# Optimization experiments

Hardware: AMD Instinct MI355X
Metric: run time of the kernel (lower is better)

The kernel has to match this reference:

```python
import jax, jax.numpy as jnp
import numpy as np

NUM_KEYS = 128          # int(sqrt(num_cdmoe_experts)) = sqrt(16384)
TOP_K = 8               # num_cdmoe_experts_per_head
NUM_HEADS = 4           # num_cdmoe_heads


def setup_inputs() -> dict:
    key = jax.random.key(0)
    ks = jax.random.split(key, 8)
    b, t, d = 1, 2048, 1024
    inter = 2048
    E, h, ret = 16384, NUM_HEADS, 64
    s = 0.02
    return {
        "hidden_states": jax.random.normal(ks[0], (b, t, d), jnp.float32),
        "w_queries": jax.random.normal(ks[1], (h * ret, d), jnp.float32) * s,
        "keys": jax.random.normal(ks[2], (h, NUM_KEYS, 2, ret // 2), jnp.float32) * s,
        "down_embed": jax.random.normal(ks[3], (E, d), jnp.float32) * s,
        "up_embed": jax.random.normal(ks[4], (E, d), jnp.float32) * s,
        "w_gate": jax.random.normal(ks[5], (inter, d), jnp.float32) * s,
        "w_up": jax.random.normal(ks[6], (inter, d), jnp.float32) * s,
        "w_down": jax.random.normal(ks[7], (d, inter), jnp.float32) * s,
    }


def reference(hidden_states, w_queries, keys, down_embed, up_embed, w_gate, w_up, w_down):
    b, t, d = hidden_states.shape
    h, nk, _, n = keys.shape  # (heads, num_keys, 2, retrieval_dim//2)
    k = TOP_K

    # query projection, split into the two product-key halves: (b, t, 2, h, n)
    q = (hidden_states @ w_queries.T).reshape(b, t, 2, h, n)
    # sim: (2, b, t, h, num_keys)
    sim = jnp.einsum("btphn,hkpn->pbthk", q, keys)

    # per-codebook top-k
    sx, ix = jax.lax.top_k(sim[0], k)  # (b, t, h, k)
    sy, iy = jax.lax.top_k(sim[1], k)

    # cartesian combine: (b, t, h, k*k)
    all_scores = (sx[..., :, None] + sy[..., None, :]).reshape(b, t, h, k * k)
    all_idx = (ix[..., :, None] * nk + iy[..., None, :]).reshape(b, t, h, k * k)

    scores, pos = jax.lax.top_k(all_scores, k)          # (b, t, h, k)
    indices = jnp.take_along_axis(all_idx, pos, axis=-1)  # expert ids in [0, nk*nk)

    de = down_embed[indices]  # (b, t, h, k, d)
    ue = up_embed[indices]    # (b, t, h, k, d)

    ew = jnp.einsum("btd,bthkd->bthk", hidden_states, de)
    ew = jax.nn.silu(ew) * jax.nn.softmax(scores, axis=-1)
    experts_states = jnp.einsum("bthk,bthkd->btd", ew, ue)

    # dense (inherited DogeMLP) path
    mlp = (jax.nn.silu(hidden_states @ w_gate.T) * (hidden_states @ w_up.T)) @ w_down.T
    return mlp + experts_states
```

## Files before the change

kernel.cpp:

```cpp
#include <hip/hip_runtime.h>
#include <hip/hip_bf16.h>
#include <math.h>


#define TOKENS 2048
#define DIM    1024
#define INTER  2048
#define NKEYS  128
#define TOPK   8
#define HEADS  4
#define NINF  -3.4e38f

typedef unsigned short ushort_t;
typedef __attribute__((ext_vector_type(8))) short bf16x8;
typedef __attribute__((ext_vector_type(4))) float f32x4;

__device__ __forceinline__ float bf2f(ushort_t u) {
    unsigned int x = (unsigned int)u << 16;
    float f; __builtin_memcpy(&f, &x, 4); return f;
}
__device__ __forceinline__ ushort_t f2bf_rne(float f) {
    unsigned int x; __builtin_memcpy(&x, &f, 4);
    x += 0x7fffu + ((x >> 16) & 1u);
    return (ushort_t)(x >> 16);
}
__device__ __forceinline__ void gload_lds16(const void* g, void* l) {
    __builtin_amdgcn_global_load_lds(
        (const __attribute__((address_space(1))) unsigned int*)g,
        (__attribute__((address_space(3))) unsigned int*)l, 16, 0, 0);
}

__global__ __launch_bounds__(256) void convert_all(
    const float* __restrict__ h,  const float* __restrict__ wq,
    const float* __restrict__ wg, const float* __restrict__ wu,
    const float* __restrict__ wd,
    ushort_t* __restrict__ hb,  ushort_t* __restrict__ wqb,
    ushort_t* __restrict__ wgb, ushort_t* __restrict__ wub,
    ushort_t* __restrict__ wdb) {
    const int i = blockIdx.x * 256 + threadIdx.x;
    const float* src; ushort_t* dst; int off;
    if      (i <  262144) { src = h;  dst = hb;  off = i; }
    else if (i <  294912) { src = wq; dst = wqb; off = i - 262144; }
    else if (i <  557056) { src = wg; dst = wgb; off = i - 294912; }
    else if (i <  819200) { src = wu; dst = wub; off = i - 557056; }
    else                  { src = wd; dst = wdb; off = i - 819200; }
    const float4* p = (const float4*)src + (size_t)off * 2;
    const float4 a = p[0], b = p[1];
    uint4 o;
    o.x = (unsigned)f2bf_rne(a.x) | ((unsigned)f2bf_rne(a.y) << 16);
    o.y = (unsigned)f2bf_rne(a.z) | ((unsigned)f2bf_rne(a.w) << 16);
    o.z = (unsigned)f2bf_rne(b.x) | ((unsigned)f2bf_rne(b.y) << 16);
    o.w = (unsigned)f2bf_rne(b.z) | ((unsigned)f2bf_rne(b.w) << 16);
    ((uint4*)dst)[off] = o;
}

template<int BM, int BN, int WR, int WC, int FM, int FN, int EPI>
__global__ __launch_bounds__(256) void mfma_gemm(const ushort_t* __restrict__ A,
                                                 const ushort_t* __restrict__ B,
                                                 const void* __restrict__ extra,
                                                 void* __restrict__ Cout,
                                                 int M, int N, int K) {
    static_assert(WR * WC == 4 && WR * FM * 16 == BM && WC * FN * 16 == BN, "geom");
    __shared__ ushort_t As[BM * 32];
    __shared__ ushort_t Bs[BN * 32];
    const int tid = threadIdx.x;
    const int w = tid >> 6, lane = tid & 63;
    const int wr = w / WC, wc = w % WC;
    const int m0 = blockIdx.y * BM, n0 = blockIdx.x * BN;

    const int srow = (w << 4) + (lane >> 2);
    const int scol = (lane & 3) << 3;
    const ushort_t* Ag = &A[(size_t)(m0 + srow) * K + scol];
    const ushort_t* Bg = &B[(size_t)(n0 + srow) * K + scol];
    ushort_t* Al = &As[w << 9];
    ushort_t* Bl = &Bs[w << 9];

    const int frow = lane & 15;
    const int fcol = (lane >> 4) << 3;
    const ushort_t* Afr = &As[(size_t)(wr * FM * 16 + frow) * 32 + fcol];
    const ushort_t* Bfr = &Bs[(size_t)(wc * FN * 16 + frow) * 32 + fcol];

    f32x4 acc[FM][FN];
#pragma unroll
    for (int i = 0; i < FM; ++i)
#pragma unroll
        for (int j = 0; j < FN; ++j) acc[i][j] = (f32x4){0.f, 0.f, 0.f, 0.f};

    for (int k0 = 0; k0 < K; k0 += 32) {
        __syncthreads();
#pragma unroll
        for (int i = 0; i < BM / 64; ++i)
            gload_lds16(Ag + (size_t)i * 64 * K + k0, Al + i * 2048);
#pragma unroll
        for (int i = 0; i < BN / 64; ++i)
            gload_lds16(Bg + (size_t)i * 64 * K + k0, Bl + i * 2048);
        __syncthreads();

        bf16x8 af[FM], bfv[FN];
#pragma unroll
        for (int i = 0; i < FM; ++i) af[i] = *(const bf16x8*)(Afr + i * 512);
#pragma unroll
        for (int j = 0; j < FN; ++j) bfv[j] = *(const bf16x8*)(Bfr + j * 512);
#pragma unroll
        for (int i = 0; i < FM; ++i)
#pragma unroll
            for (int j = 0; j < FN; ++j)
                acc[i][j] = __builtin_amdgcn_mfma_f32_16x16x32_bf16(
                    af[i], bfv[j], acc[i][j], 0, 0, 0);
    }

    const int crow0 = m0 + wr * FM * 16 + ((lane >> 4) << 2);
    const int ccol0 = n0 + wc * FN * 16 + (lane & 15);
#pragma unroll
    for (int i = 0; i < FM; ++i)
#pragma unroll
        for (int j = 0; j < FN; ++j)
#pragma unroll
            for (int r = 0; r < 4; ++r) {
                const size_t off = (size_t)(crow0 + i * 16 + r) * N + ccol0 + j * 16;
                float v = acc[i][j][r];
                if (EPI == 1) {
                    const float gg = bf2f(((const ushort_t*)extra)[off]);
                    v *= gg / (1.f + __expf(-gg));
                    ((ushort_t*)Cout)[off] = f2bf_rne(v);
                } else if (EPI == 2) {
                    ((float*)Cout)[off] = v + ((const float*)extra)[off];
                } else if (EPI == 3) {
                    ((ushort_t*)Cout)[off] = f2bf_rne(v);
                } else {
                    ((float*)Cout)[off] = v;
                }
            }
}

__global__ __launch_bounds__(256) void silu_mul_inplace(const ushort_t* __restrict__ g,
                                                        ushort_t* __restrict__ u) {
    const int i = blockIdx.x * 256 + threadIdx.x;
    const uint4 gv = ((const uint4*)g)[i];
    const uint4 uv = ((const uint4*)u)[i];
    const unsigned gw[4] = {gv.x, gv.y, gv.z, gv.w};
    const unsigned uw[4] = {uv.x, uv.y, uv.z, uv.w};
    unsigned ow[4];
#pragma unroll
    for (int j = 0; j < 4; ++j) {
        const float g0 = bf2f((ushort_t)(gw[j] & 0xffff));
        const float g1 = bf2f((ushort_t)(gw[j] >> 16));
        const float u0 = bf2f((ushort_t)(uw[j] & 0xffff));
        const float u1 = bf2f((ushort_t)(uw[j] >> 16));
        const float v0 = g0 / (1.f + __expf(-g0)) * u0;
        const float v1 = g1 / (1.f + __expf(-g1)) * u1;
        ow[j] = (unsigned)f2bf_rne(v0) | ((unsigned)f2bf_rne(v1) << 16);
    }
    ((uint4*)u)[i] = (uint4){ow[0], ow[1], ow[2], ow[3]};
}

__device__ __forceinline__ void topk_body(int t, const float* __restrict__ q,
                                          const float* __restrict__ keys,
                                          int* __restrict__ eidx,
                                          float* __restrict__ ewgt) {
    const int head = threadIdx.x >> 6;
    const int lane = threadIdx.x & 63;

    const float4* qx = (const float4*)&q[(size_t)t * 256 + head * 32];
    const float4* qy = (const float4*)&q[(size_t)t * 256 + 128 + head * 32];
    float4 qxv[8], qyv[8];
#pragma unroll
    for (int n = 0; n < 8; ++n) { qxv[n] = qx[n]; qyv[n] = qy[n]; }

    float cx0, cx1, cy0, cy1;
    {
        float s[4];
#pragma unroll
        for (int j = 0; j < 2; ++j) {
            const int k = 2 * lane + j;
            const float4* kx = (const float4*)&keys[(size_t)(((head << 7) | k) * 2 + 0) * 32];
            const float4* ky = (const float4*)&keys[(size_t)(((head << 7) | k) * 2 + 1) * 32];
            float sx = 0.f, sy = 0.f;
#pragma unroll
            for (int n = 0; n < 8; ++n) {
                const float4 a = qxv[n], b = kx[n];
                sx += a.x * b.x + a.y * b.y + a.z * b.z + a.w * b.w;
                const float4 c = qyv[n], d = ky[n];
                sy += c.x * d.x + c.y * d.y + c.z * d.z + c.w * d.w;
            }
            s[j * 2] = sx; s[j * 2 + 1] = sy;
        }
        cx0 = s[0]; cy0 = s[1]; cx1 = s[2]; cy1 = s[3];
    }

    float sx_mine = NINF, sy_mine = NINF;
    int sxi_mine = 0, syi_mine = 0;
    {
        float c0 = cx0, c1 = cx1;
#pragma unroll
        for (int it = 0; it < TOPK; ++it) {
            float bv; int bi;
            if (c1 > c0) { bv = c1; bi = 2 * lane + 1; } else { bv = c0; bi = 2 * lane; }
#pragma unroll
            for (int m = 1; m < 64; m <<= 1) {
                const float ov = __shfl_xor(bv, m);
                const int   oi = __shfl_xor(bi, m);
                if (ov > bv || (ov == bv && oi < bi)) { bv = ov; bi = oi; }
            }
            if (lane == it) { sx_mine = bv; sxi_mine = bi; }
            if (bi == 2 * lane) c0 = NINF;
            else if (bi == 2 * lane + 1) c1 = NINF;
        }
    }
    {
        float c0 = cy0, c1 = cy1;
#pragma unroll
        for (int it = 0; it < TOPK; ++it) {
            float bv; int bi;
            if (c1 > c0) { bv = c1; bi = 2 * lane + 1; } else { bv = c0; bi = 2 * lane; }
#pragma unroll
            for (int m = 1; m < 64; m <<= 1) {
                const float ov = __shfl_xor(bv, m);
                const int   oi = __shfl_xor(bi, m);
                if (ov > bv || (ov == bv && oi < bi)) { bv = ov; bi = oi; }
            }
            if (lane == it) { sy_mine = bv; syi_mine = bi; }
            if (bi == 2 * lane) c0 = NINF;
            else if (bi == 2 * lane + 1) c1 = NINF;
        }
    }

    const float sa = __shfl(sx_mine, lane >> 3);
    const int   ia = __shfl(sxi_mine, lane >> 3);
    const float sb = __shfl(sy_mine, lane & 7);
    const int   ib = __shfl(syi_mine, lane & 7);
    float cv = sa + sb;
    const int ci = ia * NKEYS + ib;

    float fs_mine = NINF; int fi_mine = 0;
#pragma unroll
    for (int it = 0; it < TOPK; ++it) {
        float bv = cv; int bp = lane; int bx = ci;
#pragma unroll
        for (int m = 1; m < 64; m <<= 1) {
            const float ov = __shfl_xor(bv, m);
            const int   op = __shfl_xor(bp, m);
            const int   ox = __shfl_xor(bx, m);
            if (ov > bv || (ov == bv && op < bp)) { bv = ov; bp = op; bx = ox; }
        }
        if (lane == it) { fs_mine = bv; fi_mine = bx; }
        if (lane == bp) cv = NINF;
    }

    float f[8];
#pragma unroll
    for (int j = 0; j < 8; ++j) f[j] = __shfl(fs_mine, j);
    float mx = f[0];
#pragma unroll
    for (int j = 1; j < 8; ++j) mx = fmaxf(mx, f[j]);
    float ssum = 0.f;
#pragma unroll
    for (int j = 0; j < 8; ++j) ssum += expf(f[j] - mx);
    if (lane < 8) {
        eidx[t * 32 + head * 8 + lane] = fi_mine;
        ewgt[t * 32 + head * 8 + lane] = expf(fs_mine - mx) / ssum;
    }
}

__global__ __launch_bounds__(256) void topk_kernel(const float* __restrict__ q,
                                                   const float* __restrict__ keys,
                                                   int* __restrict__ eidx,
                                                   float* __restrict__ ewgt) {
    topk_body(blockIdx.x, q, keys, eidx, ewgt);
}

__global__ __launch_bounds__(256) void topk_conv_kernel(
    const float* __restrict__ q, const float* __restrict__ keys,
    int* __restrict__ eidx, float* __restrict__ ewgt,
    const float* __restrict__ de_f32, const float* __restrict__ ue_f32,
    ushort_t* __restrict__ deb, ushort_t* __restrict__ ueb) {
    const int b = blockIdx.x;
    if (b < TOKENS) {
        topk_body(b, q, keys, eidx, ewgt);
        return;
    }
    const int id = b - TOKENS;
    const float* src = (id < 8192) ? de_f32 : ue_f32;
    ushort_t*    dst = (id < 8192) ? deb : ueb;
    const size_t off = (size_t)(id & 8191) * 2048 + threadIdx.x * 8;
    const float4* p = (const float4*)(src + off);
    const float4 a = p[0], bb = p[1];
    uint4 o;
    o.x = (unsigned)f2bf_rne(a.x)  | ((unsigned)f2bf_rne(a.y)  << 16);
    o.y = (unsigned)f2bf_rne(a.z)  | ((unsigned)f2bf_rne(a.w)  << 16);
    o.z = (unsigned)f2bf_rne(bb.x) | ((unsigned)f2bf_rne(bb.y) << 16);
    o.w = (unsigned)f2bf_rne(bb.z) | ((unsigned)f2bf_rne(bb.w) << 16);
    *(uint4*)(dst + off) = o;
}

template<int BF16T>
__global__ __launch_bounds__(256) void fused3_kernel(
    const ushort_t* __restrict__ A,  const ushort_t* __restrict__ Bgate,
    const ushort_t* __restrict__ Bup, ushort_t* __restrict__ G,
    ushort_t* __restrict__ U,
    const float* __restrict__ hs, const void* __restrict__ de_tab,
    const void* __restrict__ ue_tab, const int* __restrict__ eidx,
    const float* __restrict__ ewgt, float* __restrict__ estate) {
    __shared__ __align__(16) char smem[16896];
    const int b = blockIdx.x;
    const int tid = threadIdx.x;
    const int w = tid >> 6, lane = tid & 63;
    const int r6 = b % 6;

    if (r6 == 2 || r6 == 5) {
        const ushort_t* B = (r6 == 2) ? Bgate : Bup;
        ushort_t*      C  = (r6 == 2) ? G : U;
        const int id = b / 6;
        const int m0 = (id >> 4) * 64, n0 = (id & 15) * 128;
        const int N = INTER, K = DIM;
        ushort_t* As = (ushort_t*)smem;
        ushort_t* Bs = (ushort_t*)(smem + 4096);
        const int wc = w;
        const int srow = (w << 4) + (lane >> 2);
        const int scol = (lane & 3) << 3;
        const ushort_t* Ag = &A[(size_t)(m0 + srow) * K + scol];
        const ushort_t* Bg = &B[(size_t)(n0 + srow) * K + scol];
        ushort_t* Al = &As[w << 9];
        ushort_t* Bl = &Bs[w << 9];
        const int frow = lane & 15;
        const int fcol = (lane >> 4) << 3;
        const ushort_t* Afr = &As[(size_t)frow * 32 + fcol];
        const ushort_t* Bfr = &Bs[(size_t)(wc * 32 + frow) * 32 + fcol];

        f32x4 acc[4][2];
#pragma unroll
        for (int i = 0; i < 4; ++i)
#pragma unroll
            for (int j = 0; j < 2; ++j) acc[i][j] = (f32x4){0.f, 0.f, 0.f, 0.f};

        for (int k0 = 0; k0 < K; k0 += 32) {
            __syncthreads();
            gload_lds16(Ag + k0, Al);
#pragma unroll
            for (int i = 0; i < 2; ++i)
                gload_lds16(Bg + (size_t)i * 64 * K + k0, Bl + i * 2048);
            __syncthreads();

            bf16x8 af[4], bfv[2];
#pragma unroll
            for (int i = 0; i < 4; ++i) af[i] = *(const bf16x8*)(Afr + i * 512);
#pragma unroll
            for (int j = 0; j < 2; ++j) bfv[j] = *(const bf16x8*)(Bfr + j * 512);
#pragma unroll
            for (int i = 0; i < 4; ++i)
#pragma unroll
                for (int j = 0; j < 2; ++j)
                    acc[i][j] = __builtin_amdgcn_mfma_f32_16x16x32_bf16(
                        af[i], bfv[j], acc[i][j], 0, 0, 0);
        }

        const int crow0 = m0 + ((lane >> 4) << 2);
        const int ccol0 = n0 + wc * 32 + (lane & 15);
#pragma unroll
        for (int i = 0; i < 4; ++i)
#pragma unroll
            for (int j = 0; j < 2; ++j)
#pragma unroll
                for (int r = 0; r < 4; ++r) {
                    const size_t off = (size_t)(crow0 + i * 16 + r) * N + ccol0 + j * 16;
                    C[off] = f2bf_rne(acc[i][j][r]);
                }
    } else {
        const int t = (b / 6) * 4 + r6 - (r6 > 2 ? 1 : 0);
        float4 (*partial)[256] = (float4(*)[256])smem;
        int*   eid = (int*)(smem + 16384);
        float* wl  = (float*)(smem + 16512);

        if (tid < 32) { eid[tid] = eidx[t * 32 + tid]; wl[tid] = ewgt[t * 32 + tid]; }

        const float4* hs4 = (const float4*)hs + (size_t)t * 256;
        float4 h[4];
#pragma unroll
        for (int i = 0; i < 4; ++i) h[i] = hs4[i * 64 + lane];
        __syncthreads();

        float4 acc[4];
#pragma unroll
        for (int i = 0; i < 4; ++i) acc[i] = (float4){0.f, 0.f, 0.f, 0.f};

        if (BF16T) {
            const ushort4* de4 = (const ushort4*)de_tab;
            const ushort4* ue4 = (const ushort4*)ue_tab;
            ushort4 d[4], u[4], nd[4], nu[4];
            {
                const size_t bb = (size_t)eid[w * 8] * 256;
#pragma unroll
                for (int i = 0; i < 4; ++i) { d[i] = de4[bb + i * 64 + lane]; u[i] = ue4[bb + i * 64 + lane]; }
            }
#pragma unroll
            for (int jj = 0; jj < 8; ++jj) {
                if (jj < 7) {
                    const size_t bb = (size_t)eid[w * 8 + jj + 1] * 256;
#pragma unroll
                    for (int i = 0; i < 4; ++i) { nd[i] = de4[bb + i * 64 + lane]; nu[i] = ue4[bb + i * 64 + lane]; }
                }
                float s = 0.f;
#pragma unroll
                for (int i = 0; i < 4; ++i)
                    s += h[i].x * bf2f(d[i].x) + h[i].y * bf2f(d[i].y)
                       + h[i].z * bf2f(d[i].z) + h[i].w * bf2f(d[i].w);
#pragma unroll
                for (int m = 1; m < 64; m <<= 1) s += __shfl_xor(s, m);
                const float c = (s / (1.f + __expf(-s))) * wl[w * 8 + jj];
#pragma unroll
                for (int i = 0; i < 4; ++i) {
                    acc[i].x += c * bf2f(u[i].x); acc[i].y += c * bf2f(u[i].y);
                    acc[i].z += c * bf2f(u[i].z); acc[i].w += c * bf2f(u[i].w);
                }
                if (jj < 7) {
#pragma unroll
                    for (int i = 0; i < 4; ++i) { d[i] = nd[i]; u[i] = nu[i]; }
                }
            }
        } else {
            const float4* de4 = (const float4*)de_tab;
            const float4* ue4 = (const float4*)ue_tab;
            float4 d[4], u[4], nd[4], nu[4];
            {
                const size_t bb = (size_t)eid[w * 8] * 256;
#pragma unroll
                for (int i = 0; i < 4; ++i) { d[i] = de4[bb + i * 64 + lane]; u[i] = ue4[bb + i * 64 + lane]; }
            }
#pragma unroll
            for (int jj = 0; jj < 8; ++jj) {
                if (jj < 7) {
                    const size_t bb = (size_t)eid[w * 8 + jj + 1] * 256;
#pragma unroll
                    for (int i = 0; i < 4; ++i) { nd[i] = de4[bb + i * 64 + lane]; nu[i] = ue4[bb + i * 64 + lane]; }
                }
                float s = 0.f;
#pragma unroll
                for (int i = 0; i < 4; ++i)
                    s += h[i].x * d[i].x + h[i].y * d[i].y + h[i].z * d[i].z + h[i].w * d[i].w;
#pragma unroll
                for (int m = 1; m < 64; m <<= 1) s += __shfl_xor(s, m);
                const float c = (s / (1.f + __expf(-s))) * wl[w * 8 + jj];
#pragma unroll
                for (int i = 0; i < 4; ++i) {
                    acc[i].x += c * u[i].x; acc[i].y += c * u[i].y;
                    acc[i].z += c * u[i].z; acc[i].w += c * u[i].w;
                }
                if (jj < 7) {
#pragma unroll
                    for (int i = 0; i < 4; ++i) { d[i] = nd[i]; u[i] = nu[i]; }
                }
            }
        }

#pragma unroll
        for (int i = 0; i < 4; ++i) partial[w][i * 64 + lane] = acc[i];
        __syncthreads();

        const float4 p0 = partial[0][tid], p1 = partial[1][tid];
        const float4 p2 = partial[2][tid], p3 = partial[3][tid];
        float4 o;
        o.x = p0.x + p1.x + p2.x + p3.x;
        o.y = p0.y + p1.y + p2.y + p3.y;
        o.z = p0.z + p1.z + p2.z + p3.z;
        o.w = p0.w + p1.w + p2.w + p3.w;
        ((float4*)estate)[(size_t)t * 256 + tid] = o;
    }
}

extern "C" void kernel_launch(void* const* d_in, const int* in_sizes, int n_in,
                              void* d_out, int out_size, void* d_ws, size_t ws_size,
                              hipStream_t stream) {
    (void)in_sizes; (void)n_in; (void)out_size;
    const float* hidden = (const float*)d_in[0];
    const float* wq     = (const float*)d_in[1];
    const float* keys   = (const float*)d_in[2];
    const float* down_e = (const float*)d_in[3];
    const float* up_e   = (const float*)d_in[4];
    const float* wgate  = (const float*)d_in[5];
    const float* wup    = (const float*)d_in[6];
    const float* wdown  = (const float*)d_in[7];
    float* out = (float*)d_out;
    char* ws = (char*)d_ws;

    ushort_t* hb  = (ushort_t*)(ws);
    ushort_t* wqb = (ushort_t*)(ws + (4u << 20));
    ushort_t* wgb = (ushort_t*)(ws + (4608u << 10));
    ushort_t* wub = (ushort_t*)(ws + (8704u << 10));
    ushort_t* wdb = (ushort_t*)(ws + (12800u << 10));
    float*    q   = (float*)   (ws + (16896u << 10));
    ushort_t* act = (ushort_t*)(ws + (18944u << 10));
    ushort_t* g   = (ushort_t*)(ws + (27136u << 10));
    float*    wgt = (float*)   (ws + (35328u << 10));
    int*     eidx = (int*)     (ws + (35584u << 10));
    ushort_t* deb = (ushort_t*)(ws + 36700160u);
    ushort_t* ueb = (ushort_t*)(ws + 70254592u);
    float* estate = out;

    const bool bf16t = ws_size >= 103809024ull;

    convert_all<<<4224, 256, 0, stream>>>(hidden, wq, wgate, wup, wdown,
                                          hb, wqb, wgb, wub, wdb);

    mfma_gemm<64, 64, 2, 2, 2, 2, 0><<<dim3(4, 32), 256, 0, stream>>>(
        hb, wqb, nullptr, q, TOKENS, 256, DIM);

    if (bf16t) {
        topk_conv_kernel<<<TOKENS + 16384, 256, 0, stream>>>(
            q, keys, eidx, wgt, down_e, up_e, deb, ueb);
        fused3_kernel<1><<<3072, 256, 0, stream>>>(
            hb, wgb, wub, g, act, hidden, deb, ueb, eidx, wgt, estate);
    } else {
        topk_kernel<<<TOKENS, 256, 0, stream>>>(q, keys, eidx, wgt);
        fused3_kernel<0><<<3072, 256, 0, stream>>>(
            hb, wgb, wub, g, act, hidden, down_e, up_e, eidx, wgt, estate);
    }

    silu_mul_inplace<<<2048, 256, 0, stream>>>(g, act);
    mfma_gemm<64, 64, 2, 2, 2, 2, 2><<<dim3(16, 32), 256, 0, stream>>>(
        act, wdb, estate, out, TOKENS, DIM, INTER);
}
```

Before: 190.9 us.

## Replace iterative shuffle-argmax top-k with rank-by-counting in shared memory

Swaps the 8-round wavefront butterfly argmax selections (for x, y and combined scores) for a rank computation: each lane counts how many shared-memory entries beat its candidates and scatters the top-8 by rank into LDS. This removes long serial chains of cross-lane shuffles. In exchange it adds LDS traffic, several block-wide barriers and a 128-wide compare loop per lane. Tie-breaking by index is kept, so the results stay the same.

```diff
diff --git a/kernel.cpp b/kernel.cpp
--- a/kernel.cpp
+++ b/kernel.cpp
@@ -158,6 +158,15 @@
                                           const float* __restrict__ keys,
                                           int* __restrict__ eidx,
                                           float* __restrict__ ewgt) {
+    __shared__ float smx[HEADS][128];
+    __shared__ float smy[HEADS][128];
+    __shared__ float txv[HEADS][8];
+    __shared__ int   txi[HEADS][8];
+    __shared__ float tyv[HEADS][8];
+    __shared__ int   tyi[HEADS][8];
+    __shared__ float comb[HEADS][64];
+    __shared__ float tfv[HEADS][8];
+    __shared__ int   tfi[HEADS][8];
     const int head = threadIdx.x >> 6;
     const int lane = threadIdx.x & 63;
 
@@ -188,68 +197,59 @@
         cx0 = s[0]; cy0 = s[1]; cx1 = s[2]; cy1 = s[3];
     }
 
-    float sx_mine = NINF, sy_mine = NINF;
-    int sxi_mine = 0, syi_mine = 0;
-    {
-        float c0 = cx0, c1 = cx1;
-#pragma unroll
-        for (int it = 0; it < TOPK; ++it) {
-            float bv; int bi;
-            if (c1 > c0) { bv = c1; bi = 2 * lane + 1; } else { bv = c0; bi = 2 * lane; }
-#pragma unroll
-            for (int m = 1; m < 64; m <<= 1) {
-                const float ov = __shfl_xor(bv, m);
-                const int   oi = __shfl_xor(bi, m);
-                if (ov > bv || (ov == bv && oi < bi)) { bv = ov; bi = oi; }
-            }
-            if (lane == it) { sx_mine = bv; sxi_mine = bi; }
-            if (bi == 2 * lane) c0 = NINF;
-            else if (bi == 2 * lane + 1) c1 = NINF;
-        }
-    }
-    {
-        float c0 = cy0, c1 = cy1;
-#pragma unroll
-        for (int it = 0; it < TOPK; ++it) {
-            float bv; int bi;
-            if (c1 > c0) { bv = c1; bi = 2 * lane + 1; } else { bv = c0; bi = 2 * lane; }
-#pragma unroll
-            for (int m = 1; m < 64; m <<= 1) {
-                const float ov = __shfl_xor(bv, m);
-                const int   oi = __shfl_xor(bi, m);
-                if (ov > bv || (ov == bv && oi < bi)) { bv = ov; bi = oi; }
-            }
-            if (lane == it) { sy_mine = bv; syi_mine = bi; }
-            if (bi == 2 * lane) c0 = NINF;
-            else if (bi == 2 * lane + 1) c1 = NINF;
-        }
-    }
-
-    const float sa = __shfl(sx_mine, lane >> 3);
-    const int   ia = __shfl(sxi_mine, lane >> 3);
-    const float sb = __shfl(sy_mine, lane & 7);
-    const int   ib = __shfl(syi_mine, lane & 7);
-    float cv = sa + sb;
-    const int ci = ia * NKEYS + ib;
-
-    float fs_mine = NINF; int fi_mine = 0;
-#pragma unroll
-    for (int it = 0; it < TOPK; ++it) {
-        float bv = cv; int bp = lane; int bx = ci;
-#pragma unroll
-        for (int m = 1; m < 64; m <<= 1) {
-            const float ov = __shfl_xor(bv, m);
-            const int   op = __shfl_xor(bp, m);
-            const int   ox = __shfl_xor(bx, m);
-            if (ov > bv || (ov == bv && op < bp)) { bv = ov; bp = op; bx = ox; }
-        }
-        if (lane == it) { fs_mine = bv; fi_mine = bx; }
-        if (lane == bp) cv = NINF;
-    }
+    const int i0 = 2 * lane, i1 = 2 * lane + 1;
+    smx[head][i0] = cx0; smx[head][i1] = cx1;
+    smy[head][i0] = cy0; smy[head][i1] = cy1;
+    __syncthreads();
+
+    int cx0r = 0, cx1r = 0, cy0r = 0, cy1r = 0;
+#pragma unroll
+    for (int j = 0; j < 128; j += 4) {
+        const float4 sx = *(const float4*)&smx[head][j];
+        cx0r += (sx.x > cx0) | ((sx.x == cx0) & (j + 0 < i0));
+        cx0r += (sx.y > cx0) | ((sx.y == cx0) & (j + 1 < i0));
+        cx0r += (sx.z > cx0) | ((sx.z == cx0) & (j + 2 < i0));
+        cx0r += (sx.w > cx0) | ((sx.w == cx0) & (j + 3 < i0));
+        cx1r += (sx.x > cx1) | ((sx.x == cx1) & (j + 0 < i1));
+        cx1r += (sx.y > cx1) | ((sx.y == cx1) & (j + 1 < i1));
+        cx1r += (sx.z > cx1) | ((sx.z == cx1) & (j + 2 < i1));
+        cx1r += (sx.w > cx1) | ((sx.w == cx1) & (j + 3 < i1));
+        const float4 sy = *(const float4*)&smy[head][j];
+        cy0r += (sy.x > cy0) | ((sy.x == cy0) & (j + 0 < i0));
+        cy0r += (sy.y > cy0) | ((sy.y == cy0) & (j + 1 < i0));
+        cy0r += (sy.z > cy0) | ((sy.z == cy0) & (j + 2 < i0));
+        cy0r += (sy.w > cy0) | ((sy.w == cy0) & (j + 3 < i0));
+        cy1r += (sy.x > cy1) | ((sy.x == cy1) & (j + 0 < i1));
+        cy1r += (sy.y > cy1) | ((sy.y == cy1) & (j + 1 < i1));
+        cy1r += (sy.z > cy1) | ((sy.z == cy1) & (j + 2 < i1));
+        cy1r += (sy.w > cy1) | ((sy.w == cy1) & (j + 3 < i1));
+    }
+    if (cx0r < TOPK) { txv[head][cx0r] = cx0; txi[head][cx0r] = i0; }
+    if (cx1r < TOPK) { txv[head][cx1r] = cx1; txi[head][cx1r] = i1; }
+    if (cy0r < TOPK) { tyv[head][cy0r] = cy0; tyi[head][cy0r] = i0; }
+    if (cy1r < TOPK) { tyv[head][cy1r] = cy1; tyi[head][cy1r] = i1; }
+    __syncthreads();
+
+    const float cv = txv[head][lane >> 3] + tyv[head][lane & 7];
+    const int   ci = txi[head][lane >> 3] * NKEYS + tyi[head][lane & 7];
+    comb[head][lane] = cv;
+    __syncthreads();
+
+    int cr = 0;
+#pragma unroll
+    for (int j = 0; j < 64; j += 4) {
+        const float4 s = *(const float4*)&comb[head][j];
+        cr += (s.x > cv) | ((s.x == cv) & (j + 0 < lane));
+        cr += (s.y > cv) | ((s.y == cv) & (j + 1 < lane));
+        cr += (s.z > cv) | ((s.z == cv) & (j + 2 < lane));
+        cr += (s.w > cv) | ((s.w == cv) & (j + 3 < lane));
+    }
+    if (cr < TOPK) { tfv[head][cr] = cv; tfi[head][cr] = ci; }
+    __syncthreads();
 
     float f[8];
 #pragma unroll
-    for (int j = 0; j < 8; ++j) f[j] = __shfl(fs_mine, j);
+    for (int j = 0; j < 8; ++j) f[j] = tfv[head][j];
     float mx = f[0];
 #pragma unroll
     for (int j = 1; j < 8; ++j) mx = fmaxf(mx, f[j]);
@@ -257,8 +257,8 @@
 #pragma unroll
     for (int j = 0; j < 8; ++j) ssum += expf(f[j] - mx);
     if (lane < 8) {
-        eidx[t * 32 + head * 8 + lane] = fi_mine;
-        ewgt[t * 32 + head * 8 + lane] = expf(fs_mine - mx) / ssum;
+        eidx[t * 32 + head * 8 + lane] = tfi[head][lane];
+        ewgt[t * 32 + head * 8 + lane] = expf(f[lane] - mx) / ssum;
     }
 }
 
```

New measurement: 303.3 us. 58.9% more time.
